# Optimization experiments

Hardware: AMD Instinct MI355X
Metric: run time of the kernel (lower is better)

The kernel has to match this reference:

```python
import jax, jax.numpy as jnp
import numpy as np

ALPHA = 0.2  # leaky relu slope

def setup_inputs() -> dict:
    key = jax.random.key(0)
    ks = jax.random.split(key, 10)
    B, N, Din, Dout = 4, 2048, 768, 768
    return {
        'h0': jax.random.normal(ks[0], (B, N, Din), jnp.float32),
        'h1': jax.random.normal(ks[1], (B, N, Din), jnp.float32),
        'node_l1': jax.random.normal(ks[2], (2 * Dout, 1), jnp.float32),
        'edge_l1': jax.random.randint(ks[3], (B, N, N), 0, 2, jnp.int32),
        'node_l2': jax.random.normal(ks[4], (2 * Dout, 1), jnp.float32),
        'edge_l2': jax.random.randint(ks[5], (B, N, N), 0, 2, jnp.int32),
        'node_l3': jax.random.normal(ks[6], (2 * Dout, 1), jnp.float32),
        'edge_l3': jax.random.randint(ks[7], (B, N, N), 0, 2, jnp.int32),
        'W': jax.random.normal(ks[8], (Din, Dout), jnp.float32) * 0.05,
        'a': jax.random.normal(ks[9], (2 * Dout, 1), jnp.float32) * 0.05,
    }

def _pair_scores(Wh0, Wh1, vec, D):
    # (concat(Wh0_i, Wh1_j) @ vec) == Wh0_i @ vec[:D] + Wh1_j @ vec[D:]
    s0 = jnp.einsum('bnd,d->bn', Wh0, vec[:D, 0])  # [B,N0]
    s1 = jnp.einsum('bnd,d->bn', Wh1, vec[D:, 0])  # [B,N1]
    return jax.nn.leaky_relu(s0[:, :, None] + s1[:, None, :], ALPHA)  # [B,N0,N1]

def reference(h0, h1, node_l1, edge_l1, node_l2, edge_l2, node_l3, edge_l3, W, a):
    D = W.shape[1]
    Wh0 = jnp.einsum('bnd,de->bne', h0, W)
    Wh1 = jnp.einsum('bnd,de->bne', h1, W)
    e = _pair_scores(Wh0, Wh1, a, D)
    att1 = jnp.where(edge_l1 > 0, _pair_scores(Wh0, Wh1, node_l1, D), 0.0)
    att2 = jnp.where(edge_l2 > 0, _pair_scores(Wh0, Wh1, node_l2, D), 0.0)
    att3 = jnp.where(edge_l3 > 0, _pair_scores(Wh0, Wh1, node_l3, D), 0.0)
    # NB: original softmax is over dim=1 (the N0 axis)
    attention = jax.nn.softmax(e + 0.01 * (att1 + att2 + att3), axis=1)
    h_prime = jnp.einsum('bij,bjd->bid', attention, Wh1)
    return jax.nn.elu(h_prime)
```

## Files before the change

kernel.cpp:

```cpp
#include <hip/hip_runtime.h>
#include <math.h>


#define B 4
#define N 2048
#define D 768
#define BN_TOT (B * N)
#define NSPLIT 64
#define ISPAN (N / NSPLIT)

constexpr float ALPHA = 0.2f;
constexpr float SCALE = 0.01f;

typedef __attribute__((ext_vector_type(8))) short bf16x8;
typedef __attribute__((ext_vector_type(4))) short short4v;
typedef __attribute__((ext_vector_type(4))) float f32x4;

__device__ __forceinline__ float leaky(float x) { return x > 0.f ? x : ALPHA * x; }

__device__ __forceinline__ void split2(float x, short& h, short& l) {
    unsigned bx = __float_as_uint(x);
    h = (short)(bx >> 16);
    float r = x - __uint_as_float(bx & 0xffff0000u);
    l = (short)(__float_as_uint(r) >> 16);
}

__device__ __forceinline__ unsigned short rne_bf16(float x) {
    unsigned bx = __float_as_uint(x);
    bx += 0x7fffu + ((bx >> 16) & 1u);
    return (unsigned short)(bx >> 16);
}
__device__ __forceinline__ float bf16f(unsigned short h) {
    return __uint_as_float(((unsigned)h) << 16);
}

__device__ __forceinline__ void gload16(const void* g, void* l) {
    __builtin_amdgcn_global_load_lds(
        (const __attribute__((address_space(1))) void*)g,
        (__attribute__((address_space(3))) void*)l, 16, 0, 0);
}

__global__ __launch_bounds__(256) void wvec_kernel(
    const float* __restrict__ W, const float* __restrict__ a,
    const float* __restrict__ n1, const float* __restrict__ n2,
    const float* __restrict__ n3, float* __restrict__ wv) {
    const int wave = threadIdx.x >> 6, lane = threadIdx.x & 63;
    const int k = blockIdx.x * 4 + wave;
    const float* wr = W + (size_t)k * D;
    float s[8] = {0.f, 0.f, 0.f, 0.f, 0.f, 0.f, 0.f, 0.f};
    #pragma unroll
    for (int t = 0; t < D / 64; ++t) {
        const int d = lane + t * 64;
        const float w = wr[d];
        s[0] = fmaf(w, a[d],      s[0]);  s[1] = fmaf(w, a[D + d],  s[1]);
        s[2] = fmaf(w, n1[d],     s[2]);  s[3] = fmaf(w, n1[D + d], s[3]);
        s[4] = fmaf(w, n2[d],     s[4]);  s[5] = fmaf(w, n2[D + d], s[5]);
        s[6] = fmaf(w, n3[d],     s[6]);  s[7] = fmaf(w, n3[D + d], s[7]);
    }
    #pragma unroll
    for (int v = 0; v < 8; ++v) {
        float x = s[v];
        #pragma unroll
        for (int off = 32; off; off >>= 1) x += __shfl_xor(x, off);
        if (lane == 0) wv[v * D + k] = x;
    }
}

__global__ __launch_bounds__(256) void svec_kernel(
    const float* __restrict__ h0, const float* __restrict__ h1,
    const float* __restrict__ wv, float* __restrict__ svec) {
    __shared__ float wvs[8 * D];
    for (int x = threadIdx.x; x < 8 * D; x += 256) wvs[x] = wv[x];
    __syncthreads();
    const int wave = threadIdx.x >> 6, lane = threadIdx.x & 63;
    const int row = blockIdx.x * 4 + wave;
    float s[8] = {0.f, 0.f, 0.f, 0.f, 0.f, 0.f, 0.f, 0.f};
    #pragma unroll
    for (int t = 0; t < D / 64; ++t) {
        const int k = lane + t * 64;
        const float w0 = h0[(size_t)row * D + k];
        const float w1 = h1[(size_t)row * D + k];
        s[0] = fmaf(w0, wvs[0 * D + k], s[0]);  s[1] = fmaf(w1, wvs[1 * D + k], s[1]);
        s[2] = fmaf(w0, wvs[2 * D + k], s[2]);  s[3] = fmaf(w1, wvs[3 * D + k], s[3]);
        s[4] = fmaf(w0, wvs[4 * D + k], s[4]);  s[5] = fmaf(w1, wvs[5 * D + k], s[5]);
        s[6] = fmaf(w0, wvs[6 * D + k], s[6]);  s[7] = fmaf(w1, wvs[7 * D + k], s[7]);
    }
    #pragma unroll
    for (int v = 0; v < 8; ++v) {
        float x = s[v];
        #pragma unroll
        for (int off = 32; off; off >>= 1) x += __shfl_xor(x, off);
        if (lane == 0) svec[v * BN_TOT + row] = x;
    }
}

__global__ __launch_bounds__(256) void colstat_kernel(
    const int* __restrict__ e1, const int* __restrict__ e2,
    const int* __restrict__ e3, const float* __restrict__ svec,
    char* __restrict__ P, float* __restrict__ pl) {
    const int b = blockIdx.z;
    const int i0 = blockIdx.y * ISPAN;
    const int j0 = blockIdx.x * 1024 + threadIdx.x * 4;
    const int bn = b * N;
    const float4 va = *(const float4*)&svec[1 * BN_TOT + bn + j0];
    const float4 v1 = *(const float4*)&svec[3 * BN_TOT + bn + j0];
    const float4 v2 = *(const float4*)&svec[5 * BN_TOT + bn + j0];
    const float4 v3 = *(const float4*)&svec[7 * BN_TOT + bn + j0];
    const float vaa[4] = {va.x, va.y, va.z, va.w};
    const float v1a[4] = {v1.x, v1.y, v1.z, v1.w};
    const float v2a[4] = {v2.x, v2.y, v2.z, v2.w};
    const float v3a[4] = {v3.x, v3.y, v3.z, v3.w};
    float l[4] = {0.f, 0.f, 0.f, 0.f};
    for (int i = i0; i < i0 + ISPAN; ++i) {
        const float ua = svec[0 * BN_TOT + bn + i];
        const float u1 = svec[2 * BN_TOT + bn + i];
        const float u2 = svec[4 * BN_TOT + bn + i];
        const float u3 = svec[6 * BN_TOT + bn + i];
        const size_t eoff = (size_t)(bn + i) * N + j0;
        const int4 m1 = *(const int4*)&e1[eoff];
        const int4 m2 = *(const int4*)&e2[eoff];
        const int4 m3 = *(const int4*)&e3[eoff];
        const int m1a[4] = {m1.x, m1.y, m1.z, m1.w};
        const int m2a[4] = {m2.x, m2.y, m2.z, m2.w};
        const int m3a[4] = {m3.x, m3.y, m3.z, m3.w};
        unsigned short pb[4];
        #pragma unroll
        for (int c = 0; c < 4; ++c) {
            float s = leaky(ua + vaa[c]);
            float at = 0.f;
            at += (m1a[c] > 0) ? leaky(u1 + v1a[c]) : 0.f;
            at += (m2a[c] > 0) ? leaky(u2 + v2a[c]) : 0.f;
            at += (m3a[c] > 0) ? leaky(u3 + v3a[c]) : 0.f;
            s = fmaf(SCALE, at, s);
            pb[c] = rne_bf16(__expf(s));
            l[c] += bf16f(pb[c]);
        }
        *(short4v*)(P + ((size_t)(bn + i) * N + j0) * 2) =
            short4v{(short)pb[0], (short)pb[1], (short)pb[2], (short)pb[3]};
    }
    *(float4*)&pl[(size_t)(b * NSPLIT + blockIdx.y) * N + j0] =
        make_float4(l[0], l[1], l[2], l[3]);
}

__global__ __launch_bounds__(256) void combine_kernel(
    const float* __restrict__ pl, float* __restrict__ tsc) {
    const int idx = blockIdx.x * 256 + threadIdx.x;
    const int b = idx >> 11, j = idx & (N - 1);
    float sum = 0.f;
    #pragma unroll
    for (int s = 0; s < NSPLIT; ++s)
        sum += pl[(size_t)(b * NSPLIT + s) * N + j];
    tsc[idx] = 1.0f / sum;
}

__global__ __launch_bounds__(256) void split_h1_kernel(
    const float* __restrict__ h1, char* __restrict__ hs1) {
    const size_t cidx = (size_t)blockIdx.x * 256 + threadIdx.x;
    float v[8];
    *(float4*)&v[0] = *(const float4*)&h1[cidx * 8];
    *(float4*)&v[4] = *(const float4*)&h1[cidx * 8 + 4];
    short h[8], l[8];
    #pragma unroll
    for (int e = 0; e < 8; ++e) split2(v[e], h[e], l[e]);
    *(bf16x8*)(hs1 + cidx * 32) = bf16x8{h[0],h[1],h[2],h[3],h[4],h[5],h[6],h[7]};
    *(bf16x8*)(hs1 + cidx * 32 + 16) = bf16x8{l[0],l[1],l[2],l[3],l[4],l[5],l[6],l[7]};
}

__global__ __launch_bounds__(256) void split_wtb_kernel(
    const float* __restrict__ W, char* __restrict__ Wtb) {
    const int cidx = blockIdx.x * 256 + threadIdx.x;
    const int n = cidx / (D / 8);
    const int k0 = (cidx % (D / 8)) * 8;
    short h[8];
    #pragma unroll
    for (int e = 0; e < 8; ++e) h[e] = (short)rne_bf16(W[(size_t)(k0 + e) * D + n]);
    *(bf16x8*)(Wtb + (size_t)cidx * 16) = bf16x8{h[0],h[1],h[2],h[3],h[4],h[5],h[6],h[7]};
}

__global__ __launch_bounds__(256, 2) void gemm_v(
    const char* __restrict__ hs1, const char* __restrict__ Wtb,
    const float* __restrict__ tsc, char* __restrict__ Vts) {
    __shared__ char lds[32768];
    const int tid = threadIdx.x, wid = tid >> 6, lane = tid & 63;
    const int row0 = blockIdx.y * 64;
    const int col0 = blockIdx.x * 128;
    const char* Asrc = hs1 + (size_t)row0 * 3072;
    const char* Bsrc = Wtb + (size_t)col0 * 1536;
    const int wr = wid >> 1, wc = wid & 1;
    const int lrow = lane & 15, kg = lane >> 4;
    f32x4 acc[2][4] = {};

    for (int kt = 0; kt < D / 64; ++kt) {
        __syncthreads();
        #pragma unroll
        for (int s = 0; s < 2; ++s) {
            const int seg = s * 4 + wid;
            const int row = seg * 8 + (lane >> 3);
            const int c = (lane & 7) ^ (row & 7);
            const char* ga = Asrc + (size_t)kt * 256 + (size_t)row * 3072 + c * 32;
            gload16(ga,      lds + seg * 1024);
            gload16(ga + 16, lds + 8192 + seg * 1024);
        }
        #pragma unroll
        for (int s = 0; s < 4; ++s) {
            const int seg = s * 4 + wid;
            const int row = seg * 8 + (lane >> 3);
            const int c = (lane & 7) ^ (row & 7);
            gload16(Bsrc + (size_t)kt * 128 + (size_t)row * 1536 + c * 16,
                    lds + 16384 + seg * 1024);
        }
        __syncthreads();
        #pragma unroll
        for (int ks = 0; ks < 2; ++ks) {
            bf16x8 ah[2], al[2], bw[4];
            #pragma unroll
            for (int m = 0; m < 2; ++m) {
                const int r = wr * 32 + m * 16 + lrow;
                const int c = (ks * 4 + kg) ^ (r & 7);
                ah[m] = *(const bf16x8*)(lds + r * 128 + c * 16);
                al[m] = *(const bf16x8*)(lds + 8192 + r * 128 + c * 16);
            }
            #pragma unroll
            for (int n = 0; n < 4; ++n) {
                const int r = wc * 64 + n * 16 + lrow;
                const int c = (ks * 4 + kg) ^ (r & 7);
                bw[n] = *(const bf16x8*)(lds + 16384 + r * 128 + c * 16);
            }
            #pragma unroll
            for (int m = 0; m < 2; ++m)
                #pragma unroll
                for (int n = 0; n < 4; ++n) {
                    acc[m][n] = __builtin_amdgcn_mfma_f32_16x16x32_bf16(ah[m], bw[n], acc[m][n], 0, 0, 0);
                    acc[m][n] = __builtin_amdgcn_mfma_f32_16x16x32_bf16(al[m], bw[n], acc[m][n], 0, 0, 0);
                }
        }
    }
    #pragma unroll
    for (int m = 0; m < 2; ++m)
        #pragma unroll
        for (int n = 0; n < 4; ++n) {
            const int rowb = row0 + wr * 32 + m * 16 + kg * 4;
            const int col = col0 + wc * 64 + n * 16 + lrow;
            const int bq = rowb >> 11, j = rowb & (N - 1);
            short h4[4], l4[4];
            #pragma unroll
            for (int r = 0; r < 4; ++r) {
                const float x = acc[m][n][r] * tsc[bq * N + j + r];
                split2(x, h4[r], l4[r]);
            }
            char* base = Vts + ((size_t)(bq * D + col)) * 8192 + (j >> 3) * 32 + (j & 7) * 2;
            *(short4v*)base        = short4v{h4[0], h4[1], h4[2], h4[3]};
            *(short4v*)(base + 16) = short4v{l4[0], l4[1], l4[2], l4[3]};
        }
}

__global__ __launch_bounds__(256, 2) void av_kernel(
    const char* __restrict__ P, const char* __restrict__ Vts,
    float* __restrict__ out) {
    __shared__ char lds[40960];
    const int tid = threadIdx.x, wid = tid >> 6, lane = tid & 63;
    const int b = blockIdx.z;
    const int i0 = blockIdx.y * 64, d0 = blockIdx.x * 128;
    const char* Asrc = P + ((size_t)(b * N + i0)) * 4096;
    const char* Bsrc = Vts + ((size_t)(b * D + d0)) * 8192;
    const int wr = wid >> 1, wc = wid & 1;
    const int lrow = lane & 15, kg = lane >> 4;
    f32x4 acc[2][4] = {};

    for (int kt = 0; kt < N / 64; ++kt) {
        __syncthreads();
        #pragma unroll
        for (int s = 0; s < 2; ++s) {
            const int seg = s * 4 + wid;
            const int row = seg * 8 + (lane >> 3);
            const int c = (lane & 7) ^ (row & 7);
            gload16(Asrc + (size_t)kt * 128 + (size_t)row * 4096 + c * 16,
                    lds + seg * 1024);
        }
        #pragma unroll
        for (int s = 0; s < 4; ++s) {
            const int seg = s * 4 + wid;
            const int row = seg * 8 + (lane >> 3);
            const int c = (lane & 7) ^ (row & 7);
            const char* gb = Bsrc + (size_t)kt * 256 + (size_t)row * 8192 + c * 32;
            gload16(gb,      lds + 8192 + seg * 1024);
            gload16(gb + 16, lds + 24576 + seg * 1024);
        }
        __syncthreads();
        #pragma unroll
        for (int ks = 0; ks < 2; ++ks) {
            bf16x8 ap[2], bh[4], bl[4];
            #pragma unroll
            for (int m = 0; m < 2; ++m) {
                const int r = wr * 32 + m * 16 + lrow;
                const int c = (ks * 4 + kg) ^ (r & 7);
                ap[m] = *(const bf16x8*)(lds + r * 128 + c * 16);
            }
            #pragma unroll
            for (int n = 0; n < 4; ++n) {
                const int r = wc * 64 + n * 16 + lrow;
                const int c = (ks * 4 + kg) ^ (r & 7);
                bh[n] = *(const bf16x8*)(lds + 8192 + r * 128 + c * 16);
                bl[n] = *(const bf16x8*)(lds + 24576 + r * 128 + c * 16);
            }
            #pragma unroll
            for (int m = 0; m < 2; ++m)
                #pragma unroll
                for (int n = 0; n < 4; ++n) {
                    acc[m][n] = __builtin_amdgcn_mfma_f32_16x16x32_bf16(ap[m], bh[n], acc[m][n], 0, 0, 0);
                    acc[m][n] = __builtin_amdgcn_mfma_f32_16x16x32_bf16(ap[m], bl[n], acc[m][n], 0, 0, 0);
                }
        }
    }
    #pragma unroll
    for (int m = 0; m < 2; ++m)
        #pragma unroll
        for (int n = 0; n < 4; ++n) {
            const int rowi = i0 + wr * 32 + m * 16 + kg * 4;
            const int col = d0 + wc * 64 + n * 16 + lrow;
            #pragma unroll
            for (int r = 0; r < 4; ++r) {
                const float x = acc[m][n][r];
                out[((size_t)(b * N + rowi + r)) * D + col] = x > 0.f ? x : expm1f(x);
            }
        }
}

extern "C" void kernel_launch(void* const* d_in, const int* in_sizes, int n_in,
                              void* d_out, int out_size, void* d_ws, size_t ws_size,
                              hipStream_t stream) {
    const float* h0  = (const float*)d_in[0];
    const float* h1  = (const float*)d_in[1];
    const float* nl1 = (const float*)d_in[2];
    const int*   e1  = (const int*)d_in[3];
    const float* nl2 = (const float*)d_in[4];
    const int*   e2  = (const int*)d_in[5];
    const float* nl3 = (const float*)d_in[6];
    const int*   e3  = (const int*)d_in[7];
    const float* W   = (const float*)d_in[8];
    const float* a   = (const float*)d_in[9];
    float* out = (float*)d_out;

    char* ws = (char*)d_ws;
    char*  P    = ws;
    char*  hs1  = ws + 33554432;
    char*  Wtb  = ws + 58720256;
    char*  Vts  = ws + 59899904;
    float* wv   = (float*)(ws + 85065728);
    float* svec = (float*)(ws + 85090304);
    float* pl   = (float*)(ws + 85352448);
    float* tsc  = (float*)(ws + 87449600);

    wvec_kernel<<<192, 256, 0, stream>>>(W, a, nl1, nl2, nl3, wv);
    svec_kernel<<<2048, 256, 0, stream>>>(h0, h1, wv, svec);
    colstat_kernel<<<dim3(2, NSPLIT, B), 256, 0, stream>>>(e1, e2, e3, svec, P, pl);
    combine_kernel<<<BN_TOT / 256, 256, 0, stream>>>(pl, tsc);
    split_h1_kernel<<<3072, 256, 0, stream>>>(h1, hs1);
    split_wtb_kernel<<<288, 256, 0, stream>>>(W, Wtb);
    gemm_v<<<dim3(6, 128), 256, 0, stream>>>(hs1, Wtb, tsc, Vts);
    av_kernel<<<dim3(6, 32, 4), 256, 0, stream>>>(P, Vts, out);
}
```

Baseline: 402.2 us.

## Fuse h1 bf16 split into svec kernel and raise column-split count

The separate split_h1 pass is folded into the svec kernel, which already reads h1, so h1 is read from memory only once. The svec loop is rewritten to use float4 loads and emits the hi/lo bf16 halves directly in the existing hs1 layout. NSPLIT goes from 64 to 256 to give colstat four times as many blocks, and its inner loop is fully unrolled. The cost is a larger partial-sum buffer (tsc is moved to make room) and more work in the combine kernel.

```diff
diff --git a/kernel.cpp b/kernel.cpp
--- a/kernel.cpp
+++ b/kernel.cpp
@@ -6,7 +6,7 @@
 #define N 2048
 #define D 768
 #define BN_TOT (B * N)
-#define NSPLIT 64
+#define NSPLIT 256
 #define ISPAN (N / NSPLIT)
 
 constexpr float ALPHA = 0.2f;
@@ -66,9 +66,10 @@
     }
 }
 
-__global__ __launch_bounds__(256) void svec_kernel(
+__global__ __launch_bounds__(256) void svec_split_kernel(
     const float* __restrict__ h0, const float* __restrict__ h1,
-    const float* __restrict__ wv, float* __restrict__ svec) {
+    const float* __restrict__ wv, float* __restrict__ svec,
+    char* __restrict__ hs1) {
     __shared__ float wvs[8 * D];
     for (int x = threadIdx.x; x < 8 * D; x += 256) wvs[x] = wv[x];
     __syncthreads();
@@ -76,14 +77,25 @@
     const int row = blockIdx.x * 4 + wave;
     float s[8] = {0.f, 0.f, 0.f, 0.f, 0.f, 0.f, 0.f, 0.f};
     #pragma unroll
-    for (int t = 0; t < D / 64; ++t) {
-        const int k = lane + t * 64;
-        const float w0 = h0[(size_t)row * D + k];
-        const float w1 = h1[(size_t)row * D + k];
-        s[0] = fmaf(w0, wvs[0 * D + k], s[0]);  s[1] = fmaf(w1, wvs[1 * D + k], s[1]);
-        s[2] = fmaf(w0, wvs[2 * D + k], s[2]);  s[3] = fmaf(w1, wvs[3 * D + k], s[3]);
-        s[4] = fmaf(w0, wvs[4 * D + k], s[4]);  s[5] = fmaf(w1, wvs[5 * D + k], s[5]);
-        s[6] = fmaf(w0, wvs[6 * D + k], s[6]);  s[7] = fmaf(w1, wvs[7 * D + k], s[7]);
+    for (int t = 0; t < 3; ++t) {
+        const int k0 = t * 256 + lane * 4;
+        const float4 a0 = *(const float4*)&h0[(size_t)row * D + k0];
+        const float4 a1 = *(const float4*)&h1[(size_t)row * D + k0];
+        #pragma unroll
+        for (int v = 0; v < 8; v += 2) {
+            const float4 w0 = *(const float4*)&wvs[v * D + k0];
+            const float4 w1 = *(const float4*)&wvs[(v + 1) * D + k0];
+            s[v]     = fmaf(a0.x, w0.x, fmaf(a0.y, w0.y,
+                       fmaf(a0.z, w0.z, fmaf(a0.w, w0.w, s[v]))));
+            s[v + 1] = fmaf(a1.x, w1.x, fmaf(a1.y, w1.y,
+                       fmaf(a1.z, w1.z, fmaf(a1.w, w1.w, s[v + 1]))));
+        }
+        short hh[4], ll[4];
+        split2(a1.x, hh[0], ll[0]); split2(a1.y, hh[1], ll[1]);
+        split2(a1.z, hh[2], ll[2]); split2(a1.w, hh[3], ll[3]);
+        char* base = hs1 + (size_t)row * 3072 + (k0 >> 3) * 32 + (k0 & 7) * 2;
+        *(short4v*)base        = short4v{hh[0], hh[1], hh[2], hh[3]};
+        *(short4v*)(base + 16) = short4v{ll[0], ll[1], ll[2], ll[3]};
     }
     #pragma unroll
     for (int v = 0; v < 8; ++v) {
@@ -111,6 +123,7 @@
     const float v2a[4] = {v2.x, v2.y, v2.z, v2.w};
     const float v3a[4] = {v3.x, v3.y, v3.z, v3.w};
     float l[4] = {0.f, 0.f, 0.f, 0.f};
+    #pragma unroll
     for (int i = i0; i < i0 + ISPAN; ++i) {
         const float ua = svec[0 * BN_TOT + bn + i];
         const float u1 = svec[2 * BN_TOT + bn + i];
@@ -147,23 +160,10 @@
     const int idx = blockIdx.x * 256 + threadIdx.x;
     const int b = idx >> 11, j = idx & (N - 1);
     float sum = 0.f;
-    #pragma unroll
+    #pragma unroll 8
     for (int s = 0; s < NSPLIT; ++s)
         sum += pl[(size_t)(b * NSPLIT + s) * N + j];
     tsc[idx] = 1.0f / sum;
-}
-
-__global__ __launch_bounds__(256) void split_h1_kernel(
-    const float* __restrict__ h1, char* __restrict__ hs1) {
-    const size_t cidx = (size_t)blockIdx.x * 256 + threadIdx.x;
-    float v[8];
-    *(float4*)&v[0] = *(const float4*)&h1[cidx * 8];
-    *(float4*)&v[4] = *(const float4*)&h1[cidx * 8 + 4];
-    short h[8], l[8];
-    #pragma unroll
-    for (int e = 0; e < 8; ++e) split2(v[e], h[e], l[e]);
-    *(bf16x8*)(hs1 + cidx * 32) = bf16x8{h[0],h[1],h[2],h[3],h[4],h[5],h[6],h[7]};
-    *(bf16x8*)(hs1 + cidx * 32 + 16) = bf16x8{l[0],l[1],l[2],l[3],l[4],l[5],l[6],l[7]};
 }
 
 __global__ __launch_bounds__(256) void split_wtb_kernel(
@@ -349,13 +349,12 @@
     float* wv   = (float*)(ws + 85065728);
     float* svec = (float*)(ws + 85090304);
     float* pl   = (float*)(ws + 85352448);
-    float* tsc  = (float*)(ws + 87449600);
+    float* tsc  = (float*)(ws + 93741056);
 
     wvec_kernel<<<192, 256, 0, stream>>>(W, a, nl1, nl2, nl3, wv);
-    svec_kernel<<<2048, 256, 0, stream>>>(h0, h1, wv, svec);
+    svec_split_kernel<<<2048, 256, 0, stream>>>(h0, h1, wv, svec, hs1);
     colstat_kernel<<<dim3(2, NSPLIT, B), 256, 0, stream>>>(e1, e2, e3, svec, P, pl);
     combine_kernel<<<BN_TOT / 256, 256, 0, stream>>>(pl, tsc);
-    split_h1_kernel<<<3072, 256, 0, stream>>>(h1, hs1);
     split_wtb_kernel<<<288, 256, 0, stream>>>(W, Wtb);
     gemm_v<<<dim3(6, 128), 256, 0, stream>>>(hs1, Wtb, tsc, Vts);
     av_kernel<<<dim3(6, 32, 4), 256, 0, stream>>>(P, Vts, out);
```

New measurement: 383.2 us. 1.05x faster.
